# Kernel tuning notes

Hardware: AMD Instinct MI355X
Metric: run time of the kernel (lower is better)

## Reference

```python
import jax, jax.numpy as jnp
import numpy as np

B, F, T, EPT, S, E, H, LVL = 16384, 512, 4, 2, 2, 256, 128, 2

def _ple_level(xs_task, x_sh, w_task, b_task, w_sh, b_sh, w_gate, b_gate, w_gsh=None, b_gsh=None):
    # xs_task: [T,B,I] per-task inputs; x_sh: [B,I] shared input
    task_out = jax.nn.relu(jnp.einsum('tbi,teio->tbeo', xs_task, w_task) + b_task[:, None])  # [T,B,EPT,E]
    sh_out = jax.nn.relu(jnp.einsum('bi,sio->bso', x_sh, w_sh) + b_sh)                       # [B,S,E]
    t = task_out.shape[0]
    experts = jnp.concatenate([task_out, jnp.broadcast_to(sh_out[None], (t,) + sh_out.shape)], axis=2)  # [T,B,EPT+S,E]
    gate = jax.nn.softmax(jnp.einsum('tbi,tig->tbg', xs_task, w_gate) + b_gate[:, None], axis=-1)
    task_next = jnp.einsum('tbg,tbge->tbe', gate, experts)  # [T,B,E]
    sh_next = None
    if w_gsh is not None:
        # all experts ordered task0_exp0, task0_exp1, task1_exp0, ..., then shared
        bsz = x_sh.shape[0]
        all_exp = jnp.concatenate([jnp.transpose(task_out, (1, 0, 2, 3)).reshape(bsz, -1, task_out.shape[-1]), sh_out], axis=1)
        gsh = jax.nn.softmax(x_sh @ w_gsh + b_gsh, axis=-1)
        sh_next = jnp.einsum('bg,bge->be', gsh, all_exp)
    return task_next, sh_next

def setup_inputs() -> dict:
    key = jax.random.key(0)
    ks = jax.random.split(key, 16)
    sc = 0.02
    d = {
        'x': jax.random.normal(ks[0], (B, F), jnp.float32),
        # level 0 (in_dim=F, has shared gate)
        'w_task0': jax.random.normal(ks[1], (T, EPT, F, E), jnp.float32) * sc,
        'b_task0': jnp.zeros((T, EPT, E), jnp.float32),
        'w_sh0': jax.random.normal(ks[2], (S, F, E), jnp.float32) * sc,
        'b_sh0': jnp.zeros((S, E), jnp.float32),
        'w_gate0': jax.random.normal(ks[3], (T, F, EPT + S), jnp.float32) * sc,
        'b_gate0': jnp.zeros((T, EPT + S), jnp.float32),
        'w_gsh0': jax.random.normal(ks[4], (F, T * EPT + S), jnp.float32) * sc,
        'b_gsh0': jnp.zeros((T * EPT + S,), jnp.float32),
        # level 1 (last; in_dim=E, no shared gate)
        'w_task1': jax.random.normal(ks[5], (T, EPT, E, E), jnp.float32) * sc,
        'b_task1': jnp.zeros((T, EPT, E), jnp.float32),
        'w_sh1': jax.random.normal(ks[6], (S, E, E), jnp.float32) * sc,
        'b_sh1': jnp.zeros((S, E), jnp.float32),
        'w_gate1': jax.random.normal(ks[7], (T, E, EPT + S), jnp.float32) * sc,
        'b_gate1': jnp.zeros((T, EPT + S), jnp.float32),
        # towers
        'w_tw': jax.random.normal(ks[8], (T, E, H), jnp.float32) * sc,
        'b_tw': jnp.zeros((T, H), jnp.float32),
        'w_out': jax.random.normal(ks[9], (T, H, 2), jnp.float32) * sc,
        'b_out': jnp.zeros((T, 2), jnp.float32),
    }
    return d

def reference(x, w_task0, b_task0, w_sh0, b_sh0, w_gate0, b_gate0, w_gsh0, b_gsh0,
              w_task1, b_task1, w_sh1, b_sh1, w_gate1, b_gate1,
              w_tw, b_tw, w_out, b_out):
    xs_task = jnp.broadcast_to(x[None], (T,) + x.shape)  # all tasks see same input at level 0
    t1, sh1 = _ple_level(xs_task, x, w_task0, b_task0, w_sh0, b_sh0, w_gate0, b_gate0, w_gsh0, b_gsh0)
    t2, _ = _ple_level(t1, sh1, w_task1, b_task1, w_sh1, b_sh1, w_gate1, b_gate1)
    h = jax.nn.relu(jnp.einsum('tbe,teh->tbh', t2, w_tw) + b_tw[:, None])
    logits = jnp.einsum('tbh,tho->tbo', h, w_out) + b_out[:, None]
    p = jax.nn.softmax(logits, axis=-1)
    return jnp.clip(p, 1e-15, 1.0 - 1e-15)  # [T,B,2]
```

## Files before the change

kernel.cpp:

```cpp
#include <hip/hip_runtime.h>

typedef unsigned short u16;
typedef __bf16 bf16x8 __attribute__((ext_vector_type(8)));
typedef float f32x4 __attribute__((ext_vector_type(4)));
typedef u16 u16x8 __attribute__((ext_vector_type(8)));
typedef u16 u16x4 __attribute__((ext_vector_type(4)));

#define B_ 16384

__device__ __forceinline__ u16 f2b(float f){
  unsigned u = __builtin_bit_cast(unsigned, f);
  u = (u + 0x7FFFu + ((u >> 16) & 1u)) >> 16;
  return (u16)u;
}
__device__ __forceinline__ float b2f(u16 v){
  return __builtin_bit_cast(float, ((unsigned)v) << 16);
}
__device__ __forceinline__ void ld8(const u16* __restrict__ p, float* f){
  u16x8 v = *(const u16x8*)p;
  #pragma unroll
  for (int j = 0; j < 8; ++j) f[j] = b2f(v[j]);
}

__device__ __forceinline__ void gload16(const u16* g, u16* lds){
  __builtin_amdgcn_global_load_lds(
      (const __attribute__((address_space(1))) unsigned int*)g,
      (__attribute__((address_space(3))) unsigned int*)lds, 16, 0, 0);
}

__device__ __forceinline__ void core32(const u16* __restrict__ A,
                                       const u16* __restrict__ Wt,
                                       int K, int m0, int n0, int nt,
                                       u16* sm, f32x4 acc[4][4])
{
  const int tid = threadIdx.x, lane = tid & 63, wave = tid >> 6;
  const int wm = ((tid >> 7) & 3) * 64;
  const int wn = ((tid >> 6) & 1) * 64;

  #pragma unroll
  for (int m = 0; m < 4; ++m)
    #pragma unroll
    for (int n = 0; n < 4; ++n) acc[m][n] = (f32x4){0.f, 0.f, 0.f, 0.f};

  const int s_    = (lane & 7) ^ ((lane >> 3) & 7);
  const int srow2 = 2 * (lane >> 3) + (s_ >> 2);
  const int sk    = (s_ & 3) * 8;
  const u16* gsrc[3];
  int gdst[3];
  #pragma unroll
  for (int i = 0; i < 3; ++i) {
    int c = wave * 3 + i;
    if (c < 16) {
      gsrc[i] = A + (size_t)(m0 + c * 16 + srow2) * K + sk;
      gdst[i] = c * 512;
    } else {
      gsrc[i] = Wt + (size_t)(n0 + (c - 16) * 16 + srow2) * K + sk;
      gdst[i] = 8192 + (c - 16) * 512;
    }
  }

  int aoff[4], boff[4];
  #pragma unroll
  for (int m = 0; m < 4; ++m) {
    int r = wm + m * 16 + (lane & 15);
    int L = r >> 1;
    int phys = (((r & 1) << 2) + (lane >> 4)) ^ (L & 7);
    aoff[m] = L * 64 + phys * 8;
  }
  #pragma unroll
  for (int n = 0; n < 4; ++n) {
    int r = wn + n * 16 + (lane & 15);
    int L = r >> 1;
    int phys = (((r & 1) << 2) + (lane >> 4)) ^ (L & 7);
    boff[n] = 8192 + L * 64 + phys * 8;
  }

  #pragma unroll
  for (int j = 0; j < 2; ++j) {
    u16* sl = sm + j * 12288;
    #pragma unroll
    for (int i = 0; i < 3; ++i) gload16(gsrc[i] + j * 32, sl + gdst[i]);
  }
  asm volatile("s_waitcnt vmcnt(3)" ::: "memory");
  __builtin_amdgcn_s_barrier();

  int cs = 0;
  for (int j = 0; j < nt; ++j) {
    if (j + 2 < nt) {
      int ns = cs + 2; ns = (ns >= 3) ? ns - 3 : ns;
      u16* sl = sm + ns * 12288;
      #pragma unroll
      for (int i = 0; i < 3; ++i) gload16(gsrc[i] + (size_t)(j + 2) * 32, sl + gdst[i]);
    }
    const u16* sa = sm + cs * 12288;
    bf16x8 av[4], bv[4];
    #pragma unroll
    for (int m = 0; m < 4; ++m) av[m] = *(const bf16x8*)(sa + aoff[m]);
    #pragma unroll
    for (int n = 0; n < 4; ++n) bv[n] = *(const bf16x8*)(sa + boff[n]);
    __builtin_amdgcn_s_setprio(1);
    #pragma unroll
    for (int m = 0; m < 4; ++m)
      #pragma unroll
      for (int n = 0; n < 4; ++n)
        acc[m][n] = __builtin_amdgcn_mfma_f32_16x16x32_bf16(av[m], bv[n], acc[m][n], 0, 0, 0);
    __builtin_amdgcn_s_setprio(0);
    if (j + 2 < nt)      asm volatile("s_waitcnt vmcnt(3)" ::: "memory");
    else if (j + 1 < nt) asm volatile("s_waitcnt vmcnt(0)" ::: "memory");
    __builtin_amdgcn_s_barrier();
    cs = (cs == 2) ? 0 : cs + 1;
  }
}


__global__ __launch_bounds__(512) void k_gemm0sh(const u16* __restrict__ xb,
    const u16* __restrict__ WT0S, const float* __restrict__ bias0s,
    u16* __restrict__ SH0E, float* __restrict__ G0L)
{
  __shared__ __align__(16) u16 sm[36864];
  f32x4 acc[4][4];
  const int bid = blockIdx.x;
  const int swz = (bid & 7) * 40 + (bid >> 3);
  const int m0 = (swz / 5) * 256, n0 = (swz % 5) * 128;
  core32(xb, WT0S, 512, m0, n0, 16, sm, acc);
  const int lane = threadIdx.x & 63;
  const int wm = ((threadIdx.x >> 7) & 3) * 64, wn = ((threadIdx.x >> 6) & 1) * 64;
  #pragma unroll
  for (int mi = 0; mi < 4; ++mi)
    #pragma unroll
    for (int ni = 0; ni < 4; ++ni) {
      int gcol = n0 + wn + ni * 16 + (lane & 15);
      float bias = bias0s[gcol];
      #pragma unroll
      for (int q = 0; q < 4; ++q) {
        int grow = m0 + wm + mi * 16 + ((lane >> 4) << 2) + q;
        float v = acc[mi][ni][q] + bias;
        if (gcol < 512)      SH0E[(size_t)grow * 512 + gcol] = f2b(fmaxf(v, 0.f));
        else if (gcol < 538) G0L[(size_t)grow * 26 + (gcol - 512)] = v;
      }
    }
}

__global__ __launch_bounds__(256) void k_softg0(const float* __restrict__ G0L,
    float* __restrict__ G0S)
{
  const int row = blockIdx.x * 256 + threadIdx.x;
  const float* l = G0L + (size_t)row * 26;
  float* o = G0S + (size_t)row * 32;
  #pragma unroll
  for (int t = 0; t < 4; ++t) {
    float l0 = l[t*4+0], l1 = l[t*4+1], l2 = l[t*4+2], l3 = l[t*4+3];
    float m = fmaxf(fmaxf(l0, l1), fmaxf(l2, l3));
    float e0 = expf(l0-m), e1 = expf(l1-m), e2 = expf(l2-m), e3 = expf(l3-m);
    float inv = 1.f / (e0 + e1 + e2 + e3);
    o[t*4+0] = e0*inv; o[t*4+1] = e1*inv; o[t*4+2] = e2*inv; o[t*4+3] = e3*inv;
  }
  float sg[10];
  float m = l[16];
  #pragma unroll
  for (int j = 1; j < 10; ++j) m = fmaxf(m, l[16+j]);
  float s = 0.f;
  #pragma unroll
  for (int j = 0; j < 10; ++j) { sg[j] = expf(l[16+j]-m); s += sg[j]; }
  float inv = 1.f / s;
  #pragma unroll
  for (int j = 0; j < 10; ++j) o[16+j] = sg[j] * inv;
}

__global__ __launch_bounds__(512) void k_gemm0t(const u16* __restrict__ xb,
    const u16* __restrict__ WT0T, const float* __restrict__ bias0t,
    const u16* __restrict__ SH0E, const float* __restrict__ G0S,
    u16* __restrict__ T1SH)
{
  __shared__ __align__(16) u16 sm[36864];
  f32x4 acc[4][4];
  const int bid = blockIdx.x;
  const int swz = (bid & 7) * 128 + (bid >> 3);
  const int m0 = (swz >> 4) * 256, n0 = (swz & 15) * 128;
  core32(xb, WT0T, 512, m0, n0, 16, sm, acc);

  const int tid = threadIdx.x, lane = tid & 63;
  const int wmIdx = (tid >> 7) & 3;
  const int wn = ((tid >> 6) & 1) * 64;
  float* lds2 = (float*)sm;
  const int ebase = n0 >> 3;

  for (int pair = 0; pair < 2; ++pair) {
    __syncthreads();
    #pragma unroll
    for (int mi2 = 0; mi2 < 2; ++mi2) {
      int mi = pair * 2 + mi2;
      #pragma unroll
      for (int ni = 0; ni < 4; ++ni) {
        int colL = wn + ni * 16 + (lane & 15);
        float bias = bias0t[n0 + colL];
        int el = colL >> 3, s2 = colL & 7;
        #pragma unroll
        for (int q = 0; q < 4; ++q) {
          int rl = wmIdx * 32 + mi2 * 16 + ((lane >> 4) << 2) + q;
          lds2[rl * 136 + el * 9 + s2] = fmaxf(acc[mi][ni][q] + bias, 0.f);
        }
      }
    }
    __syncthreads();
    const int r = tid >> 2, p = tid & 3;
    const int grow = m0 + (r >> 5) * 64 + pair * 32 + (r & 31);
    const float* gp = G0S + (size_t)grow * 32;
    u16x4 o[5];
    #pragma unroll
    for (int k = 0; k < 4; ++k) {
      int el = p * 4 + k;
      float ex[8];
      #pragma unroll
      for (int s2 = 0; s2 < 8; ++s2) ex[s2] = lds2[r * 136 + el * 9 + s2];
      int eg = ebase + el;
      float sh0v = b2f(SH0E[(size_t)grow * 512 + eg]);
      float sh1v = b2f(SH0E[(size_t)grow * 512 + 256 + eg]);
      float sha = gp[24] * sh0v + gp[25] * sh1v;
      #pragma unroll
      for (int t = 0; t < 4; ++t) {
        float v = gp[t*4+0] * ex[2*t] + gp[t*4+1] * ex[2*t+1]
                + gp[t*4+2] * sh0v    + gp[t*4+3] * sh1v;
        o[t][k] = f2b(v);
        sha += gp[16 + 2*t] * ex[2*t] + gp[17 + 2*t] * ex[2*t+1];
      }
      o[4][k] = f2b(sha);
    }
    int eg0 = ebase + p * 4;
    #pragma unroll
    for (int t = 0; t < 5; ++t)
      *(u16x4*)(T1SH + ((size_t)t * B_ + grow) * 256 + eg0) = o[t];
  }
}

__global__ __launch_bounds__(256) void k_gate1(const u16* __restrict__ T1SH,
    const float* __restrict__ WG1T, const float* __restrict__ b_gate1,
    float* __restrict__ G1S)
{
  const int b = blockIdx.x * 8 + (threadIdx.x >> 5);
  const int e0 = (threadIdx.x & 31) * 8;
  float gp[16];
  #pragma unroll
  for (int t = 0; t < 4; ++t) {
    float v[8];
    ld8(T1SH + ((size_t)t * B_ + b) * 256 + e0, v);
    #pragma unroll
    for (int gg = 0; gg < 4; ++gg) {
      const float* wv = WG1T + ((size_t)(t * 4 + gg) * 256 + e0);
      float s = 0.f;
      #pragma unroll
      for (int j = 0; j < 8; ++j) s += v[j] * wv[j];
      gp[t * 4 + gg] = s;
    }
  }
  #pragma unroll
  for (int i = 0; i < 16; ++i) {
    #pragma unroll
    for (int off = 1; off < 32; off <<= 1)
      gp[i] += __shfl_xor(gp[i], off, 32);
  }
  if ((threadIdx.x & 31) == 0) {
    float* orow = G1S + (size_t)b * 16;
    #pragma unroll
    for (int z = 0; z < 4; ++z) {
      float l0 = gp[z*4+0] + b_gate1[z*4+0];
      float l1 = gp[z*4+1] + b_gate1[z*4+1];
      float l2 = gp[z*4+2] + b_gate1[z*4+2];
      float l3 = gp[z*4+3] + b_gate1[z*4+3];
      float m = fmaxf(fmaxf(l0, l1), fmaxf(l2, l3));
      float x0 = expf(l0-m), x1 = expf(l1-m), x2 = expf(l2-m), x3 = expf(l3-m);
      float inv = 1.f / (x0 + x1 + x2 + x3);
      orow[z*4+0] = x0*inv; orow[z*4+1] = x1*inv;
      orow[z*4+2] = x2*inv; orow[z*4+3] = x3*inv;
    }
  }
}

__global__ __launch_bounds__(512) void k_gemm1(const u16* __restrict__ T1SH,
    const u16* __restrict__ Wt1, const float* __restrict__ bias1,
    u16* __restrict__ E1, u16* __restrict__ SH1E)
{
  __shared__ __align__(16) u16 sm[36864];
  f32x4 acc[4][4];
  const int bid = blockIdx.x;
  const int swz = (bid & 7) * 160 + (bid >> 3);
  const int mi_ = swz / 20, pan = swz % 20;
  const int z  = pan >> 2;
  const int n0 = (pan & 3) * 128;
  const int m0 = mi_ * 256;
  core32(T1SH + (size_t)z * B_ * 256, Wt1 + (size_t)z * 512 * 256, 256, m0, n0, 8, sm, acc);
  const int lane = threadIdx.x & 63;
  const int wm = ((threadIdx.x >> 7) & 3) * 64, wn = ((threadIdx.x >> 6) & 1) * 64;
  const float* bias = bias1 + z * 512;
  #pragma unroll
  for (int mi = 0; mi < 4; ++mi)
    #pragma unroll
    for (int ni = 0; ni < 4; ++ni) {
      int gcol = n0 + wn + ni * 16 + (lane & 15);
      float bv = bias[gcol];
      #pragma unroll
      for (int q = 0; q < 4; ++q) {
        int grow = m0 + wm + mi * 16 + ((lane >> 4) << 2) + q;
        float v = fmaxf(acc[mi][ni][q] + bv, 0.f);
        if (z < 4) E1[((size_t)z * B_ + grow) * 512 + gcol] = f2b(v);
        else       SH1E[(size_t)grow * 512 + gcol] = f2b(v);
      }
    }
}

__global__ __launch_bounds__(256) void k_tower2(const u16* __restrict__ E1,
    const u16* __restrict__ SH1E, const float* __restrict__ G1S,
    const u16* __restrict__ Wtw, const float* __restrict__ b_tw,
    const float* __restrict__ w_out, const float* __restrict__ b_out,
    float* __restrict__ out)
{
  __shared__ __align__(16) u16 sm[32768];
  __shared__ float part[2][128][2];
  f32x4 acc[4][4];
  const int z = blockIdx.z;
  const int m0 = blockIdx.x * 128;
  const int tid = threadIdx.x, lane = tid & 63, wave = tid >> 6;
  const int wm = ((tid >> 7) & 1) * 64, wn = ((tid >> 6) & 1) * 64;

  #pragma unroll
  for (int mi = 0; mi < 4; ++mi)
    #pragma unroll
    for (int ni = 0; ni < 4; ++ni) acc[mi][ni] = (f32x4){0.f, 0.f, 0.f, 0.f};

  const int srow  = lane >> 3;
  const int gslot = (lane & 7) ^ srow;
  const int koff0 = gslot * 8;

  int growA[4], adst[4], bdst[4];
  const u16* bsrc[4];
  #pragma unroll
  for (int i = 0; i < 4; ++i) {
    int c = wave * 4 + i;
    growA[i] = m0 + c * 8 + srow;
    adst[i]  = c * 512;
    bsrc[i]  = Wtw + (size_t)z * 128 * 256 + (size_t)(c * 8 + srow) * 256 + koff0;
    bdst[i]  = 8192 + c * 512;
  }
  const u16* E1z = E1 + (size_t)z * B_ * 512;

  int aoff[2][4], boff[2][4];
  #pragma unroll
  for (int kk = 0; kk < 2; ++kk) {
    #pragma unroll
    for (int m = 0; m < 4; ++m) {
      int r = wm + m * 16 + (lane & 15);
      aoff[kk][m] = r * 64 + (((kk * 4 + (lane >> 4)) ^ (r & 7)) * 8);
    }
    #pragma unroll
    for (int n = 0; n < 4; ++n) {
      int r = wn + n * 16 + (lane & 15);
      boff[kk][n] = 8192 + r * 64 + (((kk * 4 + (lane >> 4)) ^ (r & 7)) * 8);
    }
  }

  #define STAGE_T(J, BUF) do {                                                 \
    u16* buf_ = (BUF);                                                         \
    _Pragma("unroll")                                                          \
    for (int i_ = 0; i_ < 4; ++i_) {                                           \
      size_t eoff_ = (size_t)growA[i_] * 512 + (J) * 64 + koff0;               \
      u16x8 ea_ = *(const u16x8*)(E1z + eoff_);                                \
      u16x8 eb_ = *(const u16x8*)(E1z + eoff_ + 256);                          \
      u16x8 sa_ = *(const u16x8*)(SH1E + eoff_);                               \
      u16x8 sb_ = *(const u16x8*)(SH1E + eoff_ + 256);                         \
      float4 g_ = *(const float4*)(G1S + (size_t)growA[i_] * 16 + z * 4);      \
      u16x8 o_;                                                                \
      _Pragma("unroll")                                                        \
      for (int jj_ = 0; jj_ < 8; ++jj_)                                        \
        o_[jj_] = f2b(g_.x * b2f(ea_[jj_]) + g_.y * b2f(eb_[jj_])              \
                    + g_.z * b2f(sa_[jj_]) + g_.w * b2f(sb_[jj_]));            \
      *(uint4*)(buf_ + adst[i_] + lane * 8) = __builtin_bit_cast(uint4, o_);   \
      gload16(bsrc[i_] + (J) * 64, buf_ + bdst[i_]);                           \
    }                                                                          \
  } while (0)

  STAGE_T(0, sm);
  __syncthreads();

  #pragma unroll
  for (int t = 0; t < 4; ++t) {
    if (t + 1 < 4) STAGE_T(t + 1, sm + ((t + 1) & 1) * 16384);
    const u16* sa = sm + (t & 1) * 16384;
    #pragma unroll
    for (int kk = 0; kk < 2; ++kk) {
      bf16x8 av[4], bv[4];
      #pragma unroll
      for (int m = 0; m < 4; ++m) av[m] = *(const bf16x8*)(sa + aoff[kk][m]);
      #pragma unroll
      for (int n = 0; n < 4; ++n) bv[n] = *(const bf16x8*)(sa + boff[kk][n]);
      #pragma unroll
      for (int m = 0; m < 4; ++m)
        #pragma unroll
        for (int n = 0; n < 4; ++n)
          acc[m][n] = __builtin_amdgcn_mfma_f32_16x16x32_bf16(av[m], bv[n], acc[m][n], 0, 0, 0);
    }
    if (t + 1 < 4) __syncthreads();
  }
  #undef STAGE_T

  #pragma unroll
  for (int mi = 0; mi < 4; ++mi) {
    #pragma unroll
    for (int r = 0; r < 4; ++r) {
      float p0 = 0.f, p1 = 0.f;
      #pragma unroll
      for (int ni = 0; ni < 4; ++ni) {
        int col = wn + ni * 16 + (lane & 15);
        float h = fmaxf(acc[mi][ni][r] + b_tw[z * 128 + col], 0.f);
        p0 += h * w_out[(z * 128 + col) * 2 + 0];
        p1 += h * w_out[(z * 128 + col) * 2 + 1];
      }
      #pragma unroll
      for (int off = 1; off < 16; off <<= 1) {
        p0 += __shfl_xor(p0, off);
        p1 += __shfl_xor(p1, off);
      }
      if ((lane & 15) == 0) {
        int rowl = wm + mi * 16 + ((lane >> 4) << 2) + r;
        part[wn >> 6][rowl][0] = p0;
        part[wn >> 6][rowl][1] = p1;
      }
    }
  }
  __syncthreads();
  if (threadIdx.x < 128) {
    int rowl = threadIdx.x;
    float l0 = part[0][rowl][0] + part[1][rowl][0] + b_out[z * 2 + 0];
    float l1 = part[0][rowl][1] + part[1][rowl][1] + b_out[z * 2 + 1];
    float mx = fmaxf(l0, l1);
    float e0 = expf(l0 - mx), e1 = expf(l1 - mx);
    float inv = 1.f / (e0 + e1);
    float p0 = fminf(fmaxf(e0 * inv, 1e-15f), 1.0f);
    float p1 = fminf(fmaxf(e1 * inv, 1e-15f), 1.0f);
    size_t o = ((size_t)z * B_ + m0 + rowl) * 2;
    out[o] = p0; out[o + 1] = p1;
  }
}

__global__ void k_prep(const float* __restrict__ x,
    const float* __restrict__ w_task0, const float* __restrict__ b_task0,
    const float* __restrict__ w_sh0,   const float* __restrict__ b_sh0,
    const float* __restrict__ w_gate0, const float* __restrict__ b_gate0,
    const float* __restrict__ w_gsh0,  const float* __restrict__ b_gsh0,
    const float* __restrict__ w_task1, const float* __restrict__ b_task1,
    const float* __restrict__ w_sh1,   const float* __restrict__ b_sh1,
    const float* __restrict__ w_gate1, const float* __restrict__ w_tw,
    u16* __restrict__ xb, u16* __restrict__ WT0T, float* __restrict__ bias0t,
    u16* __restrict__ WT0S, float* __restrict__ bias0s,
    u16* __restrict__ Wt1, float* __restrict__ bias1,
    u16* __restrict__ Wtw, float* __restrict__ WG1T)
{
  size_t i = (size_t)blockIdx.x * 256 + threadIdx.x;
  const size_t S_X8  = (size_t)16384 * 512 / 8;
  const size_t S_T   = (size_t)2048 * 512;
  const size_t S_BT  = 2048;
  const size_t S_S   = (size_t)640 * 512;
  const size_t S_BS  = 640;
  const size_t S_WT1 = (size_t)5 * 512 * 256;
  const size_t S_B1  = 5 * 512;
  const size_t S_WTW = (size_t)4 * 128 * 256;
  const size_t S_WG1 = 4096;

  if (i < S_X8) {
    size_t o = i * 8;
    float4 a = *(const float4*)(x + o);
    float4 b = *(const float4*)(x + o + 4);
    u16x8 v;
    v[0] = f2b(a.x); v[1] = f2b(a.y); v[2] = f2b(a.z); v[3] = f2b(a.w);
    v[4] = f2b(b.x); v[5] = f2b(b.y); v[6] = f2b(b.z); v[7] = f2b(b.w);
    *(u16x8*)(xb + o) = v;
    return;
  }
  i -= S_X8;
  if (i < S_T) {
    int c = (int)(i / 512), f = (int)(i % 512);
    int te = c & 7, e = c >> 3;
    WT0T[i] = f2b(w_task0[((size_t)te * 512 + f) * 256 + e]);
    return;
  }
  i -= S_T;
  if (i < S_BT) {
    int te = (int)i & 7, e = (int)i >> 3;
    bias0t[i] = b_task0[te * 256 + e];
    return;
  }
  i -= S_BT;
  if (i < S_S) {
    int c = (int)(i / 512), f = (int)(i % 512);
    float v = 0.f;
    if (c < 512)      { int s = c >> 8, e = c & 255; v = w_sh0[((size_t)s * 512 + f) * 256 + e]; }
    else if (c < 528) { int q = c - 512; int t = q >> 2, gg = q & 3; v = w_gate0[((size_t)t * 512 + f) * 4 + gg]; }
    else if (c < 538) { v = w_gsh0[(size_t)f * 10 + (c - 528)]; }
    WT0S[i] = f2b(v);
    return;
  }
  i -= S_S;
  if (i < S_BS) {
    int c = (int)i; float v = 0.f;
    if (c < 512)      { int s = c >> 8, e = c & 255; v = b_sh0[s * 256 + e]; }
    else if (c < 528) { v = b_gate0[c - 512]; }
    else if (c < 538) { v = b_gsh0[c - 528]; }
    bias0s[c] = v;
    return;
  }
  i -= S_BS;
  if (i < S_WT1) {
    int z = (int)(i / (512 * 256)); int rem = (int)(i % (512 * 256));
    int c = rem / 256, f = rem % 256;
    float v;
    if (z < 4) { int ee = c >> 8, o = c & 255; v = w_task1[(((size_t)(z * 2 + ee)) * 256 + f) * 256 + o]; }
    else       { int s = c >> 8, o = c & 255; v = w_sh1[((size_t)s * 256 + f) * 256 + o]; }
    Wt1[i] = f2b(v);
    return;
  }
  i -= S_WT1;
  if (i < S_B1) {
    int z = (int)(i / 512); int c = (int)(i % 512);
    float v;
    if (z < 4) { int ee = c >> 8, o = c & 255; v = b_task1[(z * 2 + ee) * 256 + o]; }
    else       { int s = c >> 8, o = c & 255; v = b_sh1[s * 256 + o]; }
    bias1[(size_t)z * 512 + c] = v;
    return;
  }
  i -= S_B1;
  if (i < S_WTW) {
    int z = (int)(i / (128 * 256)); int rem = (int)(i % (128 * 256));
    int h = rem / 256, f = rem % 256;
    Wtw[i] = f2b(w_tw[((size_t)z * 256 + f) * 128 + h]);
    return;
  }
  i -= S_WTW;
  if (i < S_WG1) {
    int t = (int)(i >> 10), gg = (int)((i >> 8) & 3), e = (int)(i & 255);
    WG1T[i] = w_gate1[((size_t)t * 256 + e) * 4 + gg];
    return;
  }
}

extern "C" void kernel_launch(void* const* d_in, const int* in_sizes, int n_in,
                              void* d_out, int out_size, void* d_ws, size_t ws_size,
                              hipStream_t stream)
{
  (void)in_sizes; (void)n_in; (void)out_size; (void)ws_size;
  const float* x       = (const float*)d_in[0];
  const float* w_task0 = (const float*)d_in[1];
  const float* b_task0 = (const float*)d_in[2];
  const float* w_sh0   = (const float*)d_in[3];
  const float* b_sh0   = (const float*)d_in[4];
  const float* w_gate0 = (const float*)d_in[5];
  const float* b_gate0 = (const float*)d_in[6];
  const float* w_gsh0  = (const float*)d_in[7];
  const float* b_gsh0  = (const float*)d_in[8];
  const float* w_task1 = (const float*)d_in[9];
  const float* b_task1 = (const float*)d_in[10];
  const float* w_sh1   = (const float*)d_in[11];
  const float* b_sh1   = (const float*)d_in[12];
  const float* w_gate1 = (const float*)d_in[13];
  const float* b_gate1 = (const float*)d_in[14];
  const float* w_tw    = (const float*)d_in[15];
  const float* b_tw    = (const float*)d_in[16];
  const float* w_out   = (const float*)d_in[17];
  const float* b_out   = (const float*)d_in[18];
  float* out = (float*)d_out;

  char* ws = (char*)d_ws;
  u16*   XB    = (u16*)  (ws + 0);
  u16*   SH1E  = (u16*)  (ws + 0);
  u16*   WT0T  = (u16*)  (ws + 16777216);
  float* BIAS0T= (float*)(ws + 18874368);
  u16*   WT0S  = (u16*)  (ws + 18882560);
  float* BIAS0S= (float*)(ws + 19537920);
  u16*   WT1   = (u16*)  (ws + 19540480);
  float* BIAS1 = (float*)(ws + 20851200);
  u16*   WTW   = (u16*)  (ws + 20861440);
  float* WG1T  = (float*)(ws + 21123584);
  u16*   SH0E  = (u16*)  (ws + 21139968);
  float* G0L   = (float*)(ws + 37917184);
  float* G0S   = (float*)(ws + 39621120);
  u16*   T1SH  = (u16*)  (ws + 41718272);
  u16*   E1    = (u16*)  (ws + 83661312);
  float* G1S   = (float*)(ws + 150770176);

  k_prep<<<12581, 256, 0, stream>>>(x, w_task0, b_task0, w_sh0, b_sh0,
      w_gate0, b_gate0, w_gsh0, b_gsh0, w_task1, b_task1, w_sh1, b_sh1,
      w_gate1, w_tw,
      XB, WT0T, BIAS0T, WT0S, BIAS0S, WT1, BIAS1, WTW, WG1T);
  k_gemm0sh<<<320, 512, 0, stream>>>(XB, WT0S, BIAS0S, SH0E, G0L);
  k_softg0<<<64, 256, 0, stream>>>(G0L, G0S);
  k_gemm0t<<<1024, 512, 0, stream>>>(XB, WT0T, BIAS0T, SH0E, G0S, T1SH);
  k_gate1<<<2048, 256, 0, stream>>>(T1SH, WG1T, b_gate1, G1S);
  k_gemm1<<<1280, 512, 0, stream>>>(T1SH, WT1, BIAS1, E1, SH1E);
  k_tower2<<<dim3(128, 1, 4), 256, 0, stream>>>(E1, SH1E, G1S, WTW, b_tw, w_out, b_out, out);
}
```

Baseline: 176.6 us.

## Fuse level-0 shared-expert GEMM, gate softmax, and task GEMM into one kernel

Merges k_gemm0sh, k_softg0 and k_gemm0t into a single k_gemm0u. Each block computes a 128-row tile over its 128 task-expert columns plus the 32 matching shared-expert columns and all 32 gate-logit columns, then does the gate softmax and mixing from LDS. This removes the SH0E/G0L/G0S round trips through global memory and two launches. In exchange the x tile is reloaded for each of the 16 column groups and the shared-expert and gate columns are recomputed redundantly, giving smaller, less MFMA-efficient tiles (4x3 per wave) and more blocks.

```diff
diff --git a/kernel.cpp b/kernel.cpp
--- a/kernel.cpp
+++ b/kernel.cpp
@@ -4,7 +4,7 @@
 typedef __bf16 bf16x8 __attribute__((ext_vector_type(8)));
 typedef float f32x4 __attribute__((ext_vector_type(4)));
 typedef u16 u16x8 __attribute__((ext_vector_type(8)));
-typedef u16 u16x4 __attribute__((ext_vector_type(4)));
+typedef u16 u16x2 __attribute__((ext_vector_type(2)));
 
 #define B_ 16384
 
@@ -112,78 +112,107 @@
   }
 }
 
-
-__global__ __launch_bounds__(512) void k_gemm0sh(const u16* __restrict__ xb,
-    const u16* __restrict__ WT0S, const float* __restrict__ bias0s,
-    u16* __restrict__ SH0E, float* __restrict__ G0L)
-{
-  __shared__ __align__(16) u16 sm[36864];
-  f32x4 acc[4][4];
-  const int bid = blockIdx.x;
-  const int swz = (bid & 7) * 40 + (bid >> 3);
-  const int m0 = (swz / 5) * 256, n0 = (swz % 5) * 128;
-  core32(xb, WT0S, 512, m0, n0, 16, sm, acc);
-  const int lane = threadIdx.x & 63;
-  const int wm = ((threadIdx.x >> 7) & 3) * 64, wn = ((threadIdx.x >> 6) & 1) * 64;
-  #pragma unroll
-  for (int mi = 0; mi < 4; ++mi)
-    #pragma unroll
-    for (int ni = 0; ni < 4; ++ni) {
-      int gcol = n0 + wn + ni * 16 + (lane & 15);
-      float bias = bias0s[gcol];
-      #pragma unroll
-      for (int q = 0; q < 4; ++q) {
-        int grow = m0 + wm + mi * 16 + ((lane >> 4) << 2) + q;
-        float v = acc[mi][ni][q] + bias;
-        if (gcol < 512)      SH0E[(size_t)grow * 512 + gcol] = f2b(fmaxf(v, 0.f));
-        else if (gcol < 538) G0L[(size_t)grow * 26 + (gcol - 512)] = v;
-      }
-    }
-}
-
-__global__ __launch_bounds__(256) void k_softg0(const float* __restrict__ G0L,
-    float* __restrict__ G0S)
-{
-  const int row = blockIdx.x * 256 + threadIdx.x;
-  const float* l = G0L + (size_t)row * 26;
-  float* o = G0S + (size_t)row * 32;
-  #pragma unroll
-  for (int t = 0; t < 4; ++t) {
-    float l0 = l[t*4+0], l1 = l[t*4+1], l2 = l[t*4+2], l3 = l[t*4+3];
-    float m = fmaxf(fmaxf(l0, l1), fmaxf(l2, l3));
-    float e0 = expf(l0-m), e1 = expf(l1-m), e2 = expf(l2-m), e3 = expf(l3-m);
-    float inv = 1.f / (e0 + e1 + e2 + e3);
-    o[t*4+0] = e0*inv; o[t*4+1] = e1*inv; o[t*4+2] = e2*inv; o[t*4+3] = e3*inv;
-  }
-  float sg[10];
-  float m = l[16];
-  #pragma unroll
-  for (int j = 1; j < 10; ++j) m = fmaxf(m, l[16+j]);
-  float s = 0.f;
-  #pragma unroll
-  for (int j = 0; j < 10; ++j) { sg[j] = expf(l[16+j]-m); s += sg[j]; }
-  float inv = 1.f / s;
-  #pragma unroll
-  for (int j = 0; j < 10; ++j) o[16+j] = sg[j] * inv;
-}
-
-__global__ __launch_bounds__(512) void k_gemm0t(const u16* __restrict__ xb,
+__global__ __launch_bounds__(512) void k_gemm0u(const u16* __restrict__ xb,
     const u16* __restrict__ WT0T, const float* __restrict__ bias0t,
-    const u16* __restrict__ SH0E, const float* __restrict__ G0S,
+    const u16* __restrict__ WT0SH, const float* __restrict__ bias0sh,
+    const u16* __restrict__ WT0G, const float* __restrict__ bias0g,
     u16* __restrict__ T1SH)
 {
   __shared__ __align__(16) u16 sm[36864];
-  f32x4 acc[4][4];
+  const int tid = threadIdx.x, lane = tid & 63, wave = tid >> 6;
+  const int wm = (wave >> 2) * 64;
+  const int nw = wave & 3;
+
   const int bid = blockIdx.x;
-  const int swz = (bid & 7) * 128 + (bid >> 3);
-  const int m0 = (swz >> 4) * 256, n0 = (swz & 15) * 128;
-  core32(xb, WT0T, 512, m0, n0, 16, sm, acc);
-
-  const int tid = threadIdx.x, lane = tid & 63;
-  const int wmIdx = (tid >> 7) & 3;
-  const int wn = ((tid >> 6) & 1) * 64;
-  float* lds2 = (float*)sm;
-  const int ebase = n0 >> 3;
+  const int swz = (bid & 7) * 256 + (bid >> 3);
+  const int mt = swz >> 4, ep = swz & 15;
+  const int m0 = mt * 128;
+
+  f32x4 acc[4][3];
+  #pragma unroll
+  for (int m = 0; m < 4; ++m)
+    #pragma unroll
+    for (int n = 0; n < 3; ++n) acc[m][n] = (f32x4){0.f, 0.f, 0.f, 0.f};
+
+  const int s_    = (lane & 7) ^ ((lane >> 3) & 7);
+  const int srow2 = 2 * (lane >> 3) + (s_ >> 2);
+  const int sk    = (s_ & 3) * 8;
+  const u16* gsrc[3];
+  int gdst[3];
+  #pragma unroll
+  for (int i = 0; i < 3; ++i) {
+    int c = wave * 3 + i;
+    const u16* src;
+    if (c < 8) {
+      src = xb + (size_t)(m0 + c * 16 + srow2) * 512 + sk;
+      gdst[i] = c * 512;
+    } else {
+      int rb16 = c - 8;
+      if (rb16 < 8)        src = WT0T  + (size_t)(ep * 128 + rb16 * 16 + srow2) * 512 + sk;
+      else if (rb16 == 8)  src = WT0SH + (size_t)(ep * 16 + srow2) * 512 + sk;
+      else if (rb16 == 9)  src = WT0SH + (size_t)(256 + ep * 16 + srow2) * 512 + sk;
+      else if (rb16 < 12)  src = WT0G  + (size_t)((rb16 - 10) * 16 + srow2) * 512 + sk;
+      else                 src = WT0G  + (size_t)srow2 * 512 + sk;
+      gdst[i] = 4096 + rb16 * 512;
+    }
+    gsrc[i] = src;
+  }
+
+  int aoff[4], boff[3];
+  #pragma unroll
+  for (int m = 0; m < 4; ++m) {
+    int r = wm + m * 16 + (lane & 15);
+    int L = r >> 1;
+    int phys = (((r & 1) << 2) + (lane >> 4)) ^ (L & 7);
+    aoff[m] = L * 64 + phys * 8;
+  }
+  #pragma unroll
+  for (int n = 0; n < 3; ++n) {
+    int rb = nw * 48 + n * 16 + (lane & 15);
+    int L = rb >> 1;
+    int phys = (((rb & 1) << 2) + (lane >> 4)) ^ (L & 7);
+    boff[n] = 4096 + L * 64 + phys * 8;
+  }
+
+  #pragma unroll
+  for (int j = 0; j < 2; ++j) {
+    u16* sl = sm + j * 12288;
+    #pragma unroll
+    for (int i = 0; i < 3; ++i) gload16(gsrc[i] + j * 32, sl + gdst[i]);
+  }
+  asm volatile("s_waitcnt vmcnt(3)" ::: "memory");
+  __builtin_amdgcn_s_barrier();
+
+  int cs = 0;
+  for (int j = 0; j < 16; ++j) {
+    if (j + 2 < 16) {
+      int ns = cs + 2; ns = (ns >= 3) ? ns - 3 : ns;
+      u16* sl = sm + ns * 12288;
+      #pragma unroll
+      for (int i = 0; i < 3; ++i) gload16(gsrc[i] + (size_t)(j + 2) * 32, sl + gdst[i]);
+    }
+    const u16* sa = sm + cs * 12288;
+    bf16x8 av[4], bv[3];
+    #pragma unroll
+    for (int m = 0; m < 4; ++m) av[m] = *(const bf16x8*)(sa + aoff[m]);
+    #pragma unroll
+    for (int n = 0; n < 3; ++n) bv[n] = *(const bf16x8*)(sa + boff[n]);
+    __builtin_amdgcn_s_setprio(1);
+    #pragma unroll
+    for (int m = 0; m < 4; ++m)
+      #pragma unroll
+      for (int n = 0; n < 3; ++n)
+        acc[m][n] = __builtin_amdgcn_mfma_f32_16x16x32_bf16(av[m], bv[n], acc[m][n], 0, 0, 0);
+    __builtin_amdgcn_s_setprio(0);
+    if (j + 2 < 16)      asm volatile("s_waitcnt vmcnt(3)" ::: "memory");
+    else if (j + 1 < 16) asm volatile("s_waitcnt vmcnt(0)" ::: "memory");
+    __builtin_amdgcn_s_barrier();
+    cs = (cs == 2) ? 0 : cs + 1;
+  }
+
+  float* t_lds = (float*)sm;
+  float* s_lds = t_lds + 8256;
+  float* g_lds = t_lds + 8256 + 2112;
 
   for (int pair = 0; pair < 2; ++pair) {
     __syncthreads();
@@ -191,45 +220,72 @@
     for (int mi2 = 0; mi2 < 2; ++mi2) {
       int mi = pair * 2 + mi2;
       #pragma unroll
-      for (int ni = 0; ni < 4; ++ni) {
-        int colL = wn + ni * 16 + (lane & 15);
-        float bias = bias0t[n0 + colL];
-        int el = colL >> 3, s2 = colL & 7;
+      for (int ni = 0; ni < 3; ++ni) {
+        int c = nw * 48 + ni * 16 + (lane & 15);
+        float bias;
+        if (c < 128)      bias = bias0t[ep * 128 + c];
+        else if (c < 160) { int idx = c - 128; bias = bias0sh[(idx >> 4) * 256 + ep * 16 + (idx & 15)]; }
+        else              bias = bias0g[c - 160];
         #pragma unroll
         for (int q = 0; q < 4; ++q) {
-          int rl = wmIdx * 32 + mi2 * 16 + ((lane >> 4) << 2) + q;
-          lds2[rl * 136 + el * 9 + s2] = fmaxf(acc[mi][ni][q] + bias, 0.f);
+          int lr = (wm >> 1) + mi2 * 16 + ((lane >> 4) << 2) + q;
+          float v = acc[mi][ni][q] + bias;
+          if (c < 128)      t_lds[lr * 129 + c] = fmaxf(v, 0.f);
+          else if (c < 160) s_lds[lr * 33 + (c - 128)] = fmaxf(v, 0.f);
+          else              g_lds[lr * 33 + (c - 160)] = v;
         }
       }
     }
     __syncthreads();
-    const int r = tid >> 2, p = tid & 3;
-    const int grow = m0 + (r >> 5) * 64 + pair * 32 + (r & 31);
-    const float* gp = G0S + (size_t)grow * 32;
-    u16x4 o[5];
-    #pragma unroll
-    for (int k = 0; k < 4; ++k) {
-      int el = p * 4 + k;
-      float ex[8];
-      #pragma unroll
-      for (int s2 = 0; s2 < 8; ++s2) ex[s2] = lds2[r * 136 + el * 9 + s2];
-      int eg = ebase + el;
-      float sh0v = b2f(SH0E[(size_t)grow * 512 + eg]);
-      float sh1v = b2f(SH0E[(size_t)grow * 512 + 256 + eg]);
-      float sha = gp[24] * sh0v + gp[25] * sh1v;
+    if (tid < 64) {
+      float* gl = g_lds + tid * 33;
       #pragma unroll
       for (int t = 0; t < 4; ++t) {
-        float v = gp[t*4+0] * ex[2*t] + gp[t*4+1] * ex[2*t+1]
-                + gp[t*4+2] * sh0v    + gp[t*4+3] * sh1v;
-        o[t][k] = f2b(v);
-        sha += gp[16 + 2*t] * ex[2*t] + gp[17 + 2*t] * ex[2*t+1];
+        float l0 = gl[t*4+0], l1 = gl[t*4+1], l2 = gl[t*4+2], l3 = gl[t*4+3];
+        float m = fmaxf(fmaxf(l0, l1), fmaxf(l2, l3));
+        float e0 = expf(l0-m), e1 = expf(l1-m), e2 = expf(l2-m), e3 = expf(l3-m);
+        float inv = 1.f / (e0 + e1 + e2 + e3);
+        gl[t*4+0] = e0*inv; gl[t*4+1] = e1*inv; gl[t*4+2] = e2*inv; gl[t*4+3] = e3*inv;
       }
-      o[4][k] = f2b(sha);
-    }
-    int eg0 = ebase + p * 4;
-    #pragma unroll
-    for (int t = 0; t < 5; ++t)
-      *(u16x4*)(T1SH + ((size_t)t * B_ + grow) * 256 + eg0) = o[t];
+      float sg[10];
+      float m = gl[16];
+      #pragma unroll
+      for (int j = 1; j < 10; ++j) m = fmaxf(m, gl[16+j]);
+      float s = 0.f;
+      #pragma unroll
+      for (int j = 0; j < 10; ++j) { sg[j] = expf(gl[16+j]-m); s += sg[j]; }
+      float inv = 1.f / s;
+      #pragma unroll
+      for (int j = 0; j < 10; ++j) gl[16+j] = sg[j] * inv;
+    }
+    __syncthreads();
+    {
+      const int lr = tid >> 3, h = tid & 7;
+      const int grow = m0 + ((lr < 32) ? (pair * 32 + lr) : (64 + pair * 32 + (lr - 32)));
+      const float* gl = g_lds + lr * 33;
+      u16x2 o[5];
+      #pragma unroll
+      for (int d = 0; d < 2; ++d) {
+        int k = h * 2 + d;
+        float ex[8];
+        #pragma unroll
+        for (int te = 0; te < 8; ++te) ex[te] = t_lds[lr * 129 + k * 8 + te];
+        float sh0 = s_lds[lr * 33 + k];
+        float sh1 = s_lds[lr * 33 + 16 + k];
+        float sha = gl[24] * sh0 + gl[25] * sh1;
+        #pragma unroll
+        for (int t = 0; t < 4; ++t) {
+          float v = gl[t*4+0] * ex[2*t] + gl[t*4+1] * ex[2*t+1]
+                  + gl[t*4+2] * sh0     + gl[t*4+3] * sh1;
+          o[t][d] = f2b(v);
+          sha += gl[16 + 2*t] * ex[2*t] + gl[17 + 2*t] * ex[2*t+1];
+        }
+        o[4][d] = f2b(sha);
+      }
+      #pragma unroll
+      for (int t = 0; t < 5; ++t)
+        *(u16x2*)(T1SH + ((size_t)t * B_ + grow) * 256 + ep * 16 + h * 2) = o[t];
+    }
   }
 }
 
@@ -450,7 +506,8 @@
     const float* __restrict__ w_sh1,   const float* __restrict__ b_sh1,
     const float* __restrict__ w_gate1, const float* __restrict__ w_tw,
     u16* __restrict__ xb, u16* __restrict__ WT0T, float* __restrict__ bias0t,
-    u16* __restrict__ WT0S, float* __restrict__ bias0s,
+    u16* __restrict__ WT0SH, float* __restrict__ bias0sh,
+    u16* __restrict__ WT0G, float* __restrict__ bias0g,
     u16* __restrict__ Wt1, float* __restrict__ bias1,
     u16* __restrict__ Wtw, float* __restrict__ WG1T)
 {
@@ -458,8 +515,10 @@
   const size_t S_X8  = (size_t)16384 * 512 / 8;
   const size_t S_T   = (size_t)2048 * 512;
   const size_t S_BT  = 2048;
-  const size_t S_S   = (size_t)640 * 512;
-  const size_t S_BS  = 640;
+  const size_t S_SH  = (size_t)512 * 512;
+  const size_t S_BSH = 512;
+  const size_t S_G   = (size_t)32 * 512;
+  const size_t S_BG  = 32;
   const size_t S_WT1 = (size_t)5 * 512 * 256;
   const size_t S_B1  = 5 * 512;
   const size_t S_WTW = (size_t)4 * 128 * 256;
@@ -489,25 +548,33 @@
     return;
   }
   i -= S_BT;
-  if (i < S_S) {
-    int c = (int)(i / 512), f = (int)(i % 512);
+  if (i < S_SH) {
+    int row = (int)(i / 512), f = (int)(i % 512);
+    int s = row >> 8, e = row & 255;
+    WT0SH[i] = f2b(w_sh0[((size_t)s * 512 + f) * 256 + e]);
+    return;
+  }
+  i -= S_SH;
+  if (i < S_BSH) {
+    bias0sh[i] = b_sh0[i];
+    return;
+  }
+  i -= S_BSH;
+  if (i < S_G) {
+    int g = (int)(i / 512), f = (int)(i % 512);
     float v = 0.f;
-    if (c < 512)      { int s = c >> 8, e = c & 255; v = w_sh0[((size_t)s * 512 + f) * 256 + e]; }
-    else if (c < 528) { int q = c - 512; int t = q >> 2, gg = q & 3; v = w_gate0[((size_t)t * 512 + f) * 4 + gg]; }
-    else if (c < 538) { v = w_gsh0[(size_t)f * 10 + (c - 528)]; }
-    WT0S[i] = f2b(v);
-    return;
-  }
-  i -= S_S;
-  if (i < S_BS) {
-    int c = (int)i; float v = 0.f;
-    if (c < 512)      { int s = c >> 8, e = c & 255; v = b_sh0[s * 256 + e]; }
-    else if (c < 528) { v = b_gate0[c - 512]; }
-    else if (c < 538) { v = b_gsh0[c - 528]; }
-    bias0s[c] = v;
-    return;
-  }
-  i -= S_BS;
+    if (g < 16)      { int t = g >> 2, gg = g & 3; v = w_gate0[((size_t)t * 512 + f) * 4 + gg]; }
+    else if (g < 26) { v = w_gsh0[(size_t)f * 10 + (g - 16)]; }
+    WT0G[i] = f2b(v);
+    return;
+  }
+  i -= S_G;
+  if (i < S_BG) {
+    int g = (int)i;
+    bias0g[g] = (g < 16) ? b_gate0[g] : ((g < 26) ? b_gsh0[g - 16] : 0.f);
+    return;
+  }
+  i -= S_BG;
   if (i < S_WT1) {
     int z = (int)(i / (512 * 256)); int rem = (int)(i % (512 * 256));
     int c = rem / 256, f = rem % 256;
@@ -568,30 +635,28 @@
   float* out = (float*)d_out;
 
   char* ws = (char*)d_ws;
-  u16*   XB    = (u16*)  (ws + 0);
-  u16*   SH1E  = (u16*)  (ws + 0);
-  u16*   WT0T  = (u16*)  (ws + 16777216);
-  float* BIAS0T= (float*)(ws + 18874368);
-  u16*   WT0S  = (u16*)  (ws + 18882560);
-  float* BIAS0S= (float*)(ws + 19537920);
-  u16*   WT1   = (u16*)  (ws + 19540480);
-  float* BIAS1 = (float*)(ws + 20851200);
-  u16*   WTW   = (u16*)  (ws + 20861440);
-  float* WG1T  = (float*)(ws + 21123584);
-  u16*   SH0E  = (u16*)  (ws + 21139968);
-  float* G0L   = (float*)(ws + 37917184);
-  float* G0S   = (float*)(ws + 39621120);
-  u16*   T1SH  = (u16*)  (ws + 41718272);
-  u16*   E1    = (u16*)  (ws + 83661312);
-  float* G1S   = (float*)(ws + 150770176);
-
-  k_prep<<<12581, 256, 0, stream>>>(x, w_task0, b_task0, w_sh0, b_sh0,
+  u16*   XB     = (u16*)  (ws + 0);
+  u16*   SH1E   = (u16*)  (ws + 0);
+  u16*   WT0T   = (u16*)  (ws + 16777216);
+  float* BIAS0T = (float*)(ws + 18874368);
+  u16*   WT0SH  = (u16*)  (ws + 18882560);
+  float* BIAS0SH= (float*)(ws + 19406848);
+  u16*   WT0G   = (u16*)  (ws + 19408896);
+  float* BIAS0G = (float*)(ws + 19441664);
+  u16*   WT1    = (u16*)  (ws + 19441792);
+  float* BIAS1  = (float*)(ws + 20752512);
+  u16*   WTW    = (u16*)  (ws + 20762752);
+  float* WG1T   = (float*)(ws + 21024896);
+  u16*   T1SH   = (u16*)  (ws + 21041280);
+  u16*   E1     = (u16*)  (ws + 62984320);
+  float* G1S    = (float*)(ws + 130093184);
+
+  k_prep<<<12389, 256, 0, stream>>>(x, w_task0, b_task0, w_sh0, b_sh0,
       w_gate0, b_gate0, w_gsh0, b_gsh0, w_task1, b_task1, w_sh1, b_sh1,
       w_gate1, w_tw,
-      XB, WT0T, BIAS0T, WT0S, BIAS0S, WT1, BIAS1, WTW, WG1T);
-  k_gemm0sh<<<320, 512, 0, stream>>>(XB, WT0S, BIAS0S, SH0E, G0L);
-  k_softg0<<<64, 256, 0, stream>>>(G0L, G0S);
-  k_gemm0t<<<1024, 512, 0, stream>>>(XB, WT0T, BIAS0T, SH0E, G0S, T1SH);
+      XB, WT0T, BIAS0T, WT0SH, BIAS0SH, WT0G, BIAS0G, WT1, BIAS1, WTW, WG1T);
+  k_gemm0u<<<2048, 512, 0, stream>>>(XB, WT0T, BIAS0T, WT0SH, BIAS0SH,
+      WT0G, BIAS0G, T1SH);
   k_gate1<<<2048, 256, 0, stream>>>(T1SH, WG1T, b_gate1, G1S);
   k_gemm1<<<1280, 512, 0, stream>>>(T1SH, WT1, BIAS1, E1, SH1E);
   k_tower2<<<dim3(128, 1, 4), 256, 0, stream>>>(E1, SH1E, G1S, WTW, b_tw, w_out, b_out, out);
```

New measurement: 176.4 us. About the same (-0.1%).
